# Kernel optimization log

Hardware: AMD Instinct MI355X
Metric: run time of the kernel (lower is better)

## Reference

```python
import jax, jax.numpy as jnp
import numpy as np

TEMPERATURE = 0.05
EPS = 1e-8  # F.cosine_similarity default eps


def setup_inputs() -> dict:
    key = jax.random.key(0)
    k1, k2 = jax.random.split(key)
    N, D = 8192, 256
    return {
        "query_embeddings": jax.random.normal(k1, (N, D), dtype=jnp.float32),
        "pos_embeddings": jax.random.normal(k2, (N, D), dtype=jnp.float32),
    }


def _normalize(x):
    # matches F.cosine_similarity: x / max(||x||, eps)
    norm = jnp.sqrt(jnp.sum(x * x, axis=-1, keepdims=True))
    return x / jnp.maximum(norm, EPS)


def reference(query_embeddings, pos_embeddings):
    q = _normalize(query_embeddings)  # [N, D]
    p = _normalize(pos_embeddings)    # [N, D]
    # cosine similarity matrix via GEMM instead of (N,N,D) broadcast
    sim = jnp.einsum("nd,md->nm", q, p) / TEMPERATURE  # [N, N]
    # cross-entropy with labels = arange(N): loss_i = logsumexp(sim_i) - sim_ii
    logz = jax.nn.logsumexp(sim, axis=-1)  # [N]
    diag = jnp.diagonal(sim)               # [N]
    loss = jnp.mean(logz - diag)
    return loss
```

## Files before the change

### kernel.cpp

```cpp
#include <hip/hip_runtime.h>
#include <hip/hip_bf16.h>

#define NROWS 8192
#define DDIM  256
#define INV_TEMP 20.0f

typedef __attribute__((ext_vector_type(8))) short bf16x8;
typedef __attribute__((ext_vector_type(4))) float f32x4;

__device__ static inline void async16(const void* g, void* l) {
    __builtin_amdgcn_global_load_lds(
        (const __attribute__((address_space(1))) void*)g,
        (__attribute__((address_space(3))) void*)l, 16, 0, 0);
}

__global__ __launch_bounds__(256) void norm_diag_kernel(
    const float* __restrict__ q, const float* __restrict__ p,
    unsigned short* __restrict__ qn, unsigned short* __restrict__ pn,
    float* __restrict__ diag)
{
    const int row  = (blockIdx.x << 2) + (threadIdx.x >> 6);
    const int lane = threadIdx.x & 63;

    const float4 qv = ((const float4*)(q + (size_t)row * DDIM))[lane];
    const float4 pv = ((const float4*)(p + (size_t)row * DDIM))[lane];

    float sq = qv.x*qv.x + qv.y*qv.y + qv.z*qv.z + qv.w*qv.w;
    float sp = pv.x*pv.x + pv.y*pv.y + pv.z*pv.z + pv.w*pv.w;
    #pragma unroll
    for (int m = 1; m < 64; m <<= 1) {
        sq += __shfl_xor(sq, m);
        sp += __shfl_xor(sp, m);
    }
    const float qs = 1.0f / fmaxf(sqrtf(sq), 1e-8f);
    const float ps = 1.0f / fmaxf(sqrtf(sp), 1e-8f);

    const float qx = qv.x*qs, qy = qv.y*qs, qz = qv.z*qs, qw = qv.w*qs;
    const float px = pv.x*ps, py = pv.y*ps, pz = pv.z*ps, pw = pv.w*ps;

    float d = qx*px + qy*py + qz*pz + qw*pw;
    #pragma unroll
    for (int m = 1; m < 64; m <<= 1) d += __shfl_xor(d, m);
    if (lane == 0) diag[row] = d * INV_TEMP;

    union { unsigned short u16[4]; uint2 v; } uq, up;
    {
        __hip_bfloat16 b;
        b = __float2bfloat16(qx); uq.u16[0] = *(unsigned short*)&b;
        b = __float2bfloat16(qy); uq.u16[1] = *(unsigned short*)&b;
        b = __float2bfloat16(qz); uq.u16[2] = *(unsigned short*)&b;
        b = __float2bfloat16(qw); uq.u16[3] = *(unsigned short*)&b;
        b = __float2bfloat16(px); up.u16[0] = *(unsigned short*)&b;
        b = __float2bfloat16(py); up.u16[1] = *(unsigned short*)&b;
        b = __float2bfloat16(pz); up.u16[2] = *(unsigned short*)&b;
        b = __float2bfloat16(pw); up.u16[3] = *(unsigned short*)&b;
    }
    *(uint2*)(qn + (size_t)row * DDIM + lane * 4) = uq.v;
    *(uint2*)(pn + (size_t)row * DDIM + lane * 4) = up.v;
}

__global__ __launch_bounds__(256, 3) void simexp_kernel(
    const unsigned short* __restrict__ qn,
    const unsigned short* __restrict__ pn,
    float* __restrict__ part)
{
    __shared__ unsigned char lds[3 * 16384];

    const int tid  = threadIdx.x;
    const int lane = tid & 63;
    const int w    = tid >> 6;
    const int wr   = w >> 1;
    const int wc   = w & 1;
    const int quad = lane >> 4;
    const int l16  = lane & 15;
    const int rowbase = blockIdx.y * 128;
    const int colbase = blockIdx.x * 128;

    const unsigned short* gA0 = qn + (size_t)(rowbase + (2*w  )*16 + l16) * DDIM + quad * 8;
    const unsigned short* gA1 = qn + (size_t)(rowbase + (2*w+1)*16 + l16) * DDIM + quad * 8;
    const unsigned short* gB0 = pn + (size_t)(colbase + (2*w  )*16 + l16) * DDIM + quad * 8;
    const unsigned short* gB1 = pn + (size_t)(colbase + (2*w+1)*16 + l16) * DDIM + quad * 8;

    f32x4 acc[4][4];
    #pragma unroll
    for (int i = 0; i < 4; ++i)
        #pragma unroll
        for (int j = 0; j < 4; ++j) acc[i][j] = (f32x4)0.0f;

#define STAGE(buf, ks) do {                                             \
        unsigned char* _b = lds + (buf) * 16384;                        \
        async16(gA0 + (ks) * 32, _b +        (2*w    ) * 1024);         \
        async16(gA1 + (ks) * 32, _b +        (2*w + 1) * 1024);         \
        async16(gB0 + (ks) * 32, _b + 8192 + (2*w    ) * 1024);         \
        async16(gB1 + (ks) * 32, _b + 8192 + (2*w + 1) * 1024);         \
    } while (0)

    STAGE(0, 0);
    STAGE(1, 1);
    asm volatile("s_waitcnt vmcnt(4)" ::: "memory");
    __builtin_amdgcn_s_barrier();
    asm volatile("" ::: "memory");

    #pragma unroll
    for (int ks = 0; ks < 8; ++ks) {
        if (ks < 6) STAGE((ks + 2) % 3, ks + 2);

        const unsigned char* ba = lds + (ks % 3) * 16384;
        bf16x8 af[4], bf[4];
        #pragma unroll
        for (int i = 0; i < 4; ++i)
            af[i] = *(const bf16x8*)(ba + (wr*4 + i) * 1024 + quad * 256 + l16 * 16);
        #pragma unroll
        for (int j = 0; j < 4; ++j)
            bf[j] = *(const bf16x8*)(ba + 8192 + (wc*4 + j) * 1024 + quad * 256 + l16 * 16);

        #pragma unroll
        for (int i = 0; i < 4; ++i)
            #pragma unroll
            for (int j = 0; j < 4; ++j)
                acc[i][j] = __builtin_amdgcn_mfma_f32_16x16x32_bf16(
                    af[i], bf[j], acc[i][j], 0, 0, 0);

        if (ks < 7) {
            if (ks < 6) { asm volatile("s_waitcnt vmcnt(4)" ::: "memory"); }
            else        { asm volatile("s_waitcnt vmcnt(0)" ::: "memory"); }
            __builtin_amdgcn_s_barrier();
            asm volatile("" ::: "memory");
        }
    }
#undef STAGE

    __syncthreads();
    float* red = (float*)lds;

    #pragma unroll
    for (int i = 0; i < 4; ++i)
        #pragma unroll
        for (int r = 0; r < 4; ++r) {
            float s = __expf(acc[i][0][r] * INV_TEMP)
                    + __expf(acc[i][1][r] * INV_TEMP)
                    + __expf(acc[i][2][r] * INV_TEMP)
                    + __expf(acc[i][3][r] * INV_TEMP);
            s += __shfl_xor(s, 1);
            s += __shfl_xor(s, 2);
            s += __shfl_xor(s, 4);
            s += __shfl_xor(s, 8);
            if (l16 == 0)
                red[wc * 128 + wr * 64 + i * 16 + quad * 4 + r] = s;
        }
    __syncthreads();

    if (tid < 128)
        part[(size_t)blockIdx.x * NROWS + rowbase + tid] = red[tid] + red[128 + tid];
}

__global__ __launch_bounds__(128) void rowsum_kernel(
    const float* __restrict__ part, const float* __restrict__ diag,
    float* __restrict__ loss_part)
{
    const int row = blockIdx.x * 128 + threadIdx.x;
    float s = 0.0f;
    #pragma unroll 4
    for (int cb = 0; cb < 64; ++cb)
        s += part[(size_t)cb * NROWS + row];
    float v = logf(s) - diag[row];

    #pragma unroll
    for (int m = 1; m < 64; m <<= 1) v += __shfl_xor(v, m);
    __shared__ float wsum[2];
    if ((threadIdx.x & 63) == 0) wsum[threadIdx.x >> 6] = v;
    __syncthreads();
    if (threadIdx.x == 0) loss_part[blockIdx.x] = wsum[0] + wsum[1];
}

__global__ __launch_bounds__(64) void final_kernel(
    const float* __restrict__ loss_part, float* __restrict__ out)
{
    float v = loss_part[threadIdx.x];
    #pragma unroll
    for (int m = 1; m < 64; m <<= 1) v += __shfl_xor(v, m);
    if (threadIdx.x == 0) out[0] = v * (1.0f / NROWS);
}

extern "C" void kernel_launch(void* const* d_in, const int* in_sizes, int n_in,
                              void* d_out, int out_size, void* d_ws, size_t ws_size,
                              hipStream_t stream)
{
    const float* q = (const float*)d_in[0];
    const float* p = (const float*)d_in[1];

    char* ws = (char*)d_ws;
    unsigned short* qn   = (unsigned short*)ws;
    unsigned short* pn   = (unsigned short*)(ws + (size_t)NROWS*DDIM*2);
    float* part      = (float*)(ws + 2*(size_t)NROWS*DDIM*2);
    float* diag      = part + 64 * (size_t)NROWS;
    float* loss_part = diag + NROWS;

    norm_diag_kernel<<<NROWS/4, 256, 0, stream>>>(q, p, qn, pn, diag);

    dim3 grid(64, 64);
    simexp_kernel<<<grid, 256, 0, stream>>>(qn, pn, part);

    rowsum_kernel<<<64, 128, 0, stream>>>(part, diag, loss_part);
    final_kernel<<<1, 64, 0, stream>>>(loss_part, (float*)d_out);
}
```

Baseline: 136.5 us.

## Enlarge GEMM tiles to 256x256 with XCD-aware block swizzle and fuse final reduction

The similarity-exp kernel now uses 512-thread blocks computing 256x256 tiles, with each wave holding 8x4 MFMA accumulators. This halves the global reloads of Q/P tiles and the partial-sum traffic. Block indices are remapped so that blocks on the same XCD share row blocks, which should improve L2 reuse. The rowsum and final kernels are merged through an atomic ticket counter that the norm kernel resets, saving one launch. The cost is more registers and LDS per block (96KB LDS, 128 accumulator floats per thread), which may lower occupancy or cause spills.

```diff
diff --git a/kernel.cpp b/kernel.cpp
--- a/kernel.cpp
+++ b/kernel.cpp
@@ -17,8 +17,10 @@
 __global__ __launch_bounds__(256) void norm_diag_kernel(
     const float* __restrict__ q, const float* __restrict__ p,
     unsigned short* __restrict__ qn, unsigned short* __restrict__ pn,
-    float* __restrict__ diag)
-{
+    float* __restrict__ diag, int* __restrict__ tickets)
+{
+    if (blockIdx.x == 0 && threadIdx.x == 0) tickets[0] = 0;
+
     const int row  = (blockIdx.x << 2) + (threadIdx.x >> 6);
     const int lane = threadIdx.x & 63;
 
@@ -59,40 +61,46 @@
     *(uint2*)(pn + (size_t)row * DDIM + lane * 4) = up.v;
 }
 
-__global__ __launch_bounds__(256, 3) void simexp_kernel(
+__global__ __launch_bounds__(512, 2) void simexp_kernel(
     const unsigned short* __restrict__ qn,
     const unsigned short* __restrict__ pn,
     float* __restrict__ part)
 {
-    __shared__ unsigned char lds[3 * 16384];
+    __shared__ unsigned char lds[3 * 32768];
 
     const int tid  = threadIdx.x;
     const int lane = tid & 63;
     const int w    = tid >> 6;
-    const int wr   = w >> 1;
-    const int wc   = w & 1;
+    const int wr   = w >> 2;
+    const int wc   = w & 3;
     const int quad = lane >> 4;
     const int l16  = lane & 15;
-    const int rowbase = blockIdx.y * 128;
-    const int colbase = blockIdx.x * 128;
+
+    const int L   = blockIdx.y * 32 + blockIdx.x;
+    const int xcd = L & 7;
+    const int c   = L >> 3;
+    const int rowblk = xcd * 4 + (c & 3);
+    const int colblk = c >> 2;
+    const int rowbase = rowblk * 256;
+    const int colbase = colblk * 256;
 
     const unsigned short* gA0 = qn + (size_t)(rowbase + (2*w  )*16 + l16) * DDIM + quad * 8;
     const unsigned short* gA1 = qn + (size_t)(rowbase + (2*w+1)*16 + l16) * DDIM + quad * 8;
     const unsigned short* gB0 = pn + (size_t)(colbase + (2*w  )*16 + l16) * DDIM + quad * 8;
     const unsigned short* gB1 = pn + (size_t)(colbase + (2*w+1)*16 + l16) * DDIM + quad * 8;
 
-    f32x4 acc[4][4];
-    #pragma unroll
-    for (int i = 0; i < 4; ++i)
+    f32x4 acc[8][4];
+    #pragma unroll
+    for (int i = 0; i < 8; ++i)
         #pragma unroll
         for (int j = 0; j < 4; ++j) acc[i][j] = (f32x4)0.0f;
 
 #define STAGE(buf, ks) do {                                             \
-        unsigned char* _b = lds + (buf) * 16384;                        \
-        async16(gA0 + (ks) * 32, _b +        (2*w    ) * 1024);         \
-        async16(gA1 + (ks) * 32, _b +        (2*w + 1) * 1024);         \
-        async16(gB0 + (ks) * 32, _b + 8192 + (2*w    ) * 1024);         \
-        async16(gB1 + (ks) * 32, _b + 8192 + (2*w + 1) * 1024);         \
+        unsigned char* _b = lds + (buf) * 32768;                        \
+        async16(gA0 + (ks) * 32, _b +         (2*w    ) * 1024);        \
+        async16(gA1 + (ks) * 32, _b +         (2*w + 1) * 1024);        \
+        async16(gB0 + (ks) * 32, _b + 16384 + (2*w    ) * 1024);        \
+        async16(gB1 + (ks) * 32, _b + 16384 + (2*w + 1) * 1024);        \
     } while (0)
 
     STAGE(0, 0);
@@ -105,17 +113,17 @@
     for (int ks = 0; ks < 8; ++ks) {
         if (ks < 6) STAGE((ks + 2) % 3, ks + 2);
 
-        const unsigned char* ba = lds + (ks % 3) * 16384;
-        bf16x8 af[4], bf[4];
-        #pragma unroll
-        for (int i = 0; i < 4; ++i)
-            af[i] = *(const bf16x8*)(ba + (wr*4 + i) * 1024 + quad * 256 + l16 * 16);
+        const unsigned char* ba = lds + (ks % 3) * 32768;
+        bf16x8 af[8], bf[4];
+        #pragma unroll
+        for (int i = 0; i < 8; ++i)
+            af[i] = *(const bf16x8*)(ba + (wr*8 + i) * 1024 + quad * 256 + l16 * 16);
         #pragma unroll
         for (int j = 0; j < 4; ++j)
-            bf[j] = *(const bf16x8*)(ba + 8192 + (wc*4 + j) * 1024 + quad * 256 + l16 * 16);
-
-        #pragma unroll
-        for (int i = 0; i < 4; ++i)
+            bf[j] = *(const bf16x8*)(ba + 16384 + (wc*4 + j) * 1024 + quad * 256 + l16 * 16);
+
+        #pragma unroll
+        for (int i = 0; i < 8; ++i)
             #pragma unroll
             for (int j = 0; j < 4; ++j)
                 acc[i][j] = __builtin_amdgcn_mfma_f32_16x16x32_bf16(
@@ -134,7 +142,7 @@
     float* red = (float*)lds;
 
     #pragma unroll
-    for (int i = 0; i < 4; ++i)
+    for (int i = 0; i < 8; ++i)
         #pragma unroll
         for (int r = 0; r < 4; ++r) {
             float s = __expf(acc[i][0][r] * INV_TEMP)
@@ -146,40 +154,49 @@
             s += __shfl_xor(s, 4);
             s += __shfl_xor(s, 8);
             if (l16 == 0)
-                red[wc * 128 + wr * 64 + i * 16 + quad * 4 + r] = s;
+                red[wc * 256 + wr * 128 + i * 16 + quad * 4 + r] = s;
         }
     __syncthreads();
 
-    if (tid < 128)
-        part[(size_t)blockIdx.x * NROWS + rowbase + tid] = red[tid] + red[128 + tid];
-}
-
-__global__ __launch_bounds__(128) void rowsum_kernel(
+    if (tid < 256)
+        part[(size_t)colblk * NROWS + rowbase + tid] =
+            red[tid] + red[256 + tid] + red[512 + tid] + red[768 + tid];
+}
+
+__global__ __launch_bounds__(128) void rowsum_final_kernel(
     const float* __restrict__ part, const float* __restrict__ diag,
-    float* __restrict__ loss_part)
+    float* __restrict__ loss_part, int* __restrict__ tickets,
+    float* __restrict__ out)
 {
     const int row = blockIdx.x * 128 + threadIdx.x;
     float s = 0.0f;
     #pragma unroll 4
-    for (int cb = 0; cb < 64; ++cb)
+    for (int cb = 0; cb < 32; ++cb)
         s += part[(size_t)cb * NROWS + row];
     float v = logf(s) - diag[row];
 
     #pragma unroll
     for (int m = 1; m < 64; m <<= 1) v += __shfl_xor(v, m);
     __shared__ float wsum[2];
+    __shared__ int swin;
     if ((threadIdx.x & 63) == 0) wsum[threadIdx.x >> 6] = v;
     __syncthreads();
-    if (threadIdx.x == 0) loss_part[blockIdx.x] = wsum[0] + wsum[1];
-}
-
-__global__ __launch_bounds__(64) void final_kernel(
-    const float* __restrict__ loss_part, float* __restrict__ out)
-{
-    float v = loss_part[threadIdx.x];
-    #pragma unroll
-    for (int m = 1; m < 64; m <<= 1) v += __shfl_xor(v, m);
-    if (threadIdx.x == 0) out[0] = v * (1.0f / NROWS);
+    if (threadIdx.x == 0) {
+        __hip_atomic_store(&loss_part[blockIdx.x], wsum[0] + wsum[1],
+            __ATOMIC_RELEASE, __HIP_MEMORY_SCOPE_AGENT);
+        swin = __hip_atomic_fetch_add(&tickets[0], 1,
+                   __ATOMIC_ACQ_REL, __HIP_MEMORY_SCOPE_AGENT);
+    }
+    __syncthreads();
+    if (swin != 63) return;
+
+    if (threadIdx.x < 64) {
+        float x = __hip_atomic_load(&loss_part[threadIdx.x],
+                      __ATOMIC_RELAXED, __HIP_MEMORY_SCOPE_AGENT);
+        #pragma unroll
+        for (int m = 1; m < 64; m <<= 1) x += __shfl_xor(x, m);
+        if (threadIdx.x == 0) out[0] = x * (1.0f / NROWS);
+    }
 }
 
 extern "C" void kernel_launch(void* const* d_in, const int* in_sizes, int n_in,
@@ -193,14 +210,15 @@
     unsigned short* qn   = (unsigned short*)ws;
     unsigned short* pn   = (unsigned short*)(ws + (size_t)NROWS*DDIM*2);
     float* part      = (float*)(ws + 2*(size_t)NROWS*DDIM*2);
-    float* diag      = part + 64 * (size_t)NROWS;
+    float* diag      = part + 32 * (size_t)NROWS;
     float* loss_part = diag + NROWS;
-
-    norm_diag_kernel<<<NROWS/4, 256, 0, stream>>>(q, p, qn, pn, diag);
-
-    dim3 grid(64, 64);
-    simexp_kernel<<<grid, 256, 0, stream>>>(qn, pn, part);
-
-    rowsum_kernel<<<64, 128, 0, stream>>>(part, diag, loss_part);
-    final_kernel<<<1, 64, 0, stream>>>(loss_part, (float*)d_out);
-}
+    int*   tickets   = (int*)(loss_part + 64);
+
+    norm_diag_kernel<<<NROWS/4, 256, 0, stream>>>(q, p, qn, pn, diag, tickets);
+
+    dim3 grid(32, 32);
+    simexp_kernel<<<grid, 512, 0, stream>>>(qn, pn, part);
+
+    rowsum_final_kernel<<<64, 128, 0, stream>>>(part, diag, loss_part,
+                                                tickets, (float*)d_out);
+}
```

After: 131.1 us. 3.9% less time.
